# Optimization experiments

Hardware: AMD Instinct MI355X
Metric: run time of the kernel (lower is better)

## Reference

```python
import jax, jax.numpy as jnp
import numpy as np

N = 8192  # number of observations (rows of configuration)
D = 128   # embedding dimension


def _pair_indices(n):
    """Pair ordering of the original TF loop: for upper in 2..n-1, lower in 0..upper-1.
    (Pair (0,1) is never emitted by the original code.)"""
    counts = np.arange(2, n, dtype=np.int64)          # block u contributes u pairs
    uppers = np.repeat(counts, counts)
    starts = np.concatenate([np.zeros(1, np.int64), np.cumsum(counts)[:-1]])
    lowers = np.arange(uppers.shape[0], dtype=np.int64) - np.repeat(starts, counts)
    return lowers.astype(np.int32), uppers.astype(np.int32)


def setup_inputs() -> dict:
    key = jax.random.key(0)
    inputs = jax.random.normal(key, (N, D), dtype=jnp.float32)
    return {"inputs": inputs}


def reference(inputs):
    n = inputs.shape[0]
    lowers, uppers = _pair_indices(n)  # static (numpy) index arrays
    # trace(X^T (e_l-e_u)(e_l-e_u)^T X) == ||x_l - x_u||^2
    # Gram trick: ||x_l - x_u||^2 = ||x_l||^2 + ||x_u||^2 - 2 <x_l, x_u>
    sq = jnp.sum(inputs * inputs, axis=1)          # [n]
    gram = inputs @ inputs.T                        # [n, n]
    dists = sq[lowers] + sq[uppers] - 2.0 * gram[lowers, uppers]
    # Original TensorArray has size (n^2-n)/2 but only (n^2-n)/2 - 1 slots are
    # written (pair (0,1) is skipped); the last slot stacks as zero.
    out = jnp.concatenate([dists, jnp.zeros((1,), dists.dtype)])
    return out[None, :]  # tf.expand_dims(..., 0)
```

## Files before the change

kernel.cpp:

```cpp
#include <hip/hip_runtime.h>
#include <hip/hip_bf16.h>

#define NROWS 8192
#define DIM   128
#define NT    64
#define NBLK  (NT * (NT + 1) / 2)
#define TOTAL_OUT 33550336u

typedef short bf16x8 __attribute__((ext_vector_type(8)));
typedef float f32x4  __attribute__((ext_vector_type(4)));
typedef unsigned short u16x8 __attribute__((ext_vector_type(8)));

static __device__ inline unsigned short f32_to_bf16(float f) {
    unsigned int u = __float_as_uint(f);
    u += 0x7FFFu + ((u >> 16) & 1u);
    return (unsigned short)(u >> 16);
}

__global__ __launch_bounds__(256) void prep_kernel(const float* __restrict__ X,
                                                   unsigned short* __restrict__ Xr,
                                                   float* __restrict__ sq,
                                                   float* __restrict__ out) {
    __shared__ float sm[16][17];
    const int g = blockIdx.x;
    const int t = threadIdx.x;
    const int kk = t >> 6, lane = t & 63;
    const int lrow = lane & 15, kgrp = lane >> 4;

    const float* src = X + (size_t)(g * 16 + lrow) * DIM + (kk * 4 + kgrp) * 8;
    const float4 v0 = *reinterpret_cast<const float4*>(src);
    const float4 v1 = *reinterpret_cast<const float4*>(src + 4);

    u16x8 h;
    h[0] = f32_to_bf16(v0.x); h[1] = f32_to_bf16(v0.y);
    h[2] = f32_to_bf16(v0.z); h[3] = f32_to_bf16(v0.w);
    h[4] = f32_to_bf16(v1.x); h[5] = f32_to_bf16(v1.y);
    h[6] = f32_to_bf16(v1.z); h[7] = f32_to_bf16(v1.w);
    *reinterpret_cast<u16x8*>(Xr + ((size_t)(g * 4 + kk) * 64 + lane) * 8) = h;

    float p = v0.x * v0.x + v0.y * v0.y + v0.z * v0.z + v0.w * v0.w
            + v1.x * v1.x + v1.y * v1.y + v1.z * v1.z + v1.w * v1.w;
    sm[lrow][kk * 4 + kgrp] = p;
    __syncthreads();
    if (t < 16) {
        float s = 0.f;
        #pragma unroll
        for (int j = 0; j < 16; ++j) s += sm[t][j];
        sq[g * 16 + t] = s;
    }
    if (g == 0 && t == 0) out[TOTAL_OUT - 1] = 0.0f;
}

__global__ __launch_bounds__(256, 4) void pdist_kernel(const unsigned short* __restrict__ Xr,
                                                       const float* __restrict__ sq,
                                                       float* __restrict__ out) {
    const int t  = threadIdx.x;
    const int bt = blockIdx.x;
    int bj = (int)((sqrtf(8.0f * (float)bt + 1.0f) - 1.0f) * 0.5f);
    while ((bj + 1) * (bj + 2) / 2 <= bt) ++bj;
    while (bj * (bj + 1) / 2 > bt) --bj;
    const int bi = bt - bj * (bj + 1) / 2;

    const int wid  = t >> 6;
    const int lane = t & 63;
    const int wr   = wid >> 1;
    const int wc   = wid & 1;
    const int lrow = lane & 15;
    const int kgrp = lane >> 4;

    const bf16x8* __restrict__ F = reinterpret_cast<const bf16x8*>(Xr);
    const int gA = bi * 8 + wr * 4;
    const int gB = bj * 8 + wc * 4;

    f32x4 acc[4][4];
    const f32x4 fzero = {0.f, 0.f, 0.f, 0.f};
    #pragma unroll
    for (int m = 0; m < 4; ++m)
        #pragma unroll
        for (int n = 0; n < 4; ++n) acc[m][n] = fzero;

    bf16x8 a[2][4], b[2][4];
    #pragma unroll
    for (int m = 0; m < 4; ++m) {
        a[0][m] = F[((gA + m) * 4 + 0) * 64 + lane];
        b[0][m] = F[((gB + m) * 4 + 0) * 64 + lane];
    }
    #pragma unroll
    for (int kk = 0; kk < 4; ++kk) {
        const int cur = kk & 1, nxt = cur ^ 1;
        if (kk < 3) {
            #pragma unroll
            for (int m = 0; m < 4; ++m) {
                a[nxt][m] = F[((gA + m) * 4 + kk + 1) * 64 + lane];
                b[nxt][m] = F[((gB + m) * 4 + kk + 1) * 64 + lane];
            }
        }
        #pragma unroll
        for (int m = 0; m < 4; ++m)
            #pragma unroll
            for (int n = 0; n < 4; ++n)
                acc[m][n] = __builtin_amdgcn_mfma_f32_16x16x32_bf16(a[cur][m], b[cur][n], acc[m][n], 0, 0, 0);
    }

    const int l0 = bi * 128 + wr * 64;
    const int u0 = bj * 128 + wc * 64;
    const int rj = kgrp * 4;

    float squ[4];
    f32x4 sql[4];
    #pragma unroll
    for (int n = 0; n < 4; ++n) squ[n] = sq[u0 + n * 16 + lrow];
    #pragma unroll
    for (int m = 0; m < 4; ++m)
        sql[m] = *reinterpret_cast<const f32x4*>(sq + l0 + m * 16 + rj);

    if (bi != bj) {
        #pragma unroll
        for (int m = 0; m < 4; ++m) {
            #pragma unroll
            for (int n = 0; n < 4; ++n) {
                const int u = u0 + n * 16 + lrow;
                const size_t base = ((size_t)u * (u - 1)) / 2 - 1 + (size_t)(l0 + m * 16 + rj);
                f32x4 d;
                #pragma unroll
                for (int j = 0; j < 4; ++j) d[j] = sql[m][j] + squ[n] - 2.0f * acc[m][n][j];
                __builtin_memcpy(out + base, &d, 16);
            }
        }
    } else {
        #pragma unroll
        for (int m = 0; m < 4; ++m) {
            #pragma unroll
            for (int n = 0; n < 4; ++n) {
                const int u = u0 + n * 16 + lrow;
                #pragma unroll
                for (int j = 0; j < 4; ++j) {
                    const int l = l0 + m * 16 + rj + j;
                    if (l < u && u >= 2) {
                        out[((size_t)u * (u - 1)) / 2 - 1 + l] = sql[m][j] + squ[n] - 2.0f * acc[m][n][j];
                    }
                }
            }
        }
    }
}

extern "C" void kernel_launch(void* const* d_in, const int* in_sizes, int n_in,
                              void* d_out, int out_size, void* d_ws, size_t ws_size,
                              hipStream_t stream) {
    const float* X = (const float*)d_in[0];
    float* out = (float*)d_out;
    unsigned short* Xr = (unsigned short*)d_ws;
    float* sq = (float*)((char*)d_ws + (size_t)NROWS * DIM * 2);

    prep_kernel<<<NROWS / 16, 256, 0, stream>>>(X, Xr, sq, out);
    pdist_kernel<<<NBLK, 256, 0, stream>>>(Xr, sq, out);
}
```

Baseline: 54.08 us.

## Stage output tile in LDS for coalesced row stores with 256x64 tiles

Changes the block tiling from 128x128 to 256 lower rows by 64 upper columns and stages the distance tile through XOR-swizzled shared memory. Each wave can then write contiguous 1 KB segments of each packed output row instead of scattered 16-byte chunks. The aim is better write coalescing on a kernel dominated by its roughly 134 MB output. The cost is 32 KB of LDS per block plus two barriers, which may limit occupancy, and the diagonal tiles now use a simpler masked store path.

```diff
diff --git a/kernel.cpp b/kernel.cpp
--- a/kernel.cpp
+++ b/kernel.cpp
@@ -3,9 +3,8 @@
 
 #define NROWS 8192
 #define DIM   128
-#define NT    64
-#define NBLK  (NT * (NT + 1) / 2)
 #define TOTAL_OUT 33550336u
+#define NBLK2 2112
 
 typedef short bf16x8 __attribute__((ext_vector_type(8)));
 typedef float f32x4  __attribute__((ext_vector_type(4)));
@@ -15,6 +14,11 @@
     unsigned int u = __float_as_uint(f);
     u += 0x7FFFu + ((u >> 16) & 1u);
     return (unsigned short)(u >> 16);
+}
+
+static __device__ inline int cumtiles(int b) {
+    int q = b >> 2, r = b & 3;
+    return 2 * q * (q + 1) + r * (q + 1);
 }
 
 __global__ __launch_bounds__(256) void prep_kernel(const float* __restrict__ X,
@@ -54,23 +58,25 @@
 __global__ __launch_bounds__(256, 4) void pdist_kernel(const unsigned short* __restrict__ Xr,
                                                        const float* __restrict__ sq,
                                                        float* __restrict__ out) {
+    __shared__ f32x4 smC[32 * 64];
+
     const int t  = threadIdx.x;
     const int bt = blockIdx.x;
-    int bj = (int)((sqrtf(8.0f * (float)bt + 1.0f) - 1.0f) * 0.5f);
-    while ((bj + 1) * (bj + 2) / 2 <= bt) ++bj;
-    while (bj * (bj + 1) / 2 > bt) --bj;
-    const int bi = bt - bj * (bj + 1) / 2;
+    int bj = (int)sqrtf(8.0f * (float)bt + 1.0f);
+    if (bj > 127) bj = 127;
+    while (cumtiles(bj) > bt) --bj;
+    while (bj < 127 && cumtiles(bj + 1) <= bt) ++bj;
+    const int bi = bt - cumtiles(bj);
 
     const int wid  = t >> 6;
     const int lane = t & 63;
-    const int wr   = wid >> 1;
-    const int wc   = wid & 1;
+    const int wr   = wid;
     const int lrow = lane & 15;
     const int kgrp = lane >> 4;
 
     const bf16x8* __restrict__ F = reinterpret_cast<const bf16x8*>(Xr);
-    const int gA = bi * 8 + wr * 4;
-    const int gB = bj * 8 + wc * 4;
+    const int gA = bi * 16 + wr * 4;
+    const int gB = bj * 4;
 
     f32x4 acc[4][4];
     const f32x4 fzero = {0.f, 0.f, 0.f, 0.f};
@@ -102,9 +108,9 @@
                 acc[m][n] = __builtin_amdgcn_mfma_f32_16x16x32_bf16(a[cur][m], b[cur][n], acc[m][n], 0, 0, 0);
     }
 
-    const int l0 = bi * 128 + wr * 64;
-    const int u0 = bj * 128 + wc * 64;
-    const int rj = kgrp * 4;
+    const int u0  = bj * 64;
+    const int l0w = bi * 256 + wr * 64;
+    const bool diag = (bi == (bj >> 2));
 
     float squ[4];
     f32x4 sql[4];
@@ -112,33 +118,42 @@
     for (int n = 0; n < 4; ++n) squ[n] = sq[u0 + n * 16 + lrow];
     #pragma unroll
     for (int m = 0; m < 4; ++m)
-        sql[m] = *reinterpret_cast<const f32x4*>(sq + l0 + m * 16 + rj);
+        sql[m] = *reinterpret_cast<const f32x4*>(sq + l0w + m * 16 + kgrp * 4);
 
-    if (bi != bj) {
+    #pragma unroll
+    for (int h = 0; h < 2; ++h) {
+        if (h) __syncthreads();
         #pragma unroll
         for (int m = 0; m < 4; ++m) {
             #pragma unroll
-            for (int n = 0; n < 4; ++n) {
-                const int u = u0 + n * 16 + lrow;
-                const size_t base = ((size_t)u * (u - 1)) / 2 - 1 + (size_t)(l0 + m * 16 + rj);
+            for (int nn = 0; nn < 2; ++nn) {
+                const int n = 2 * h + nn;
+                const int u_loc = nn * 16 + lrow;
+                const int c = wr * 16 + m * 4 + kgrp;
                 f32x4 d;
                 #pragma unroll
                 for (int j = 0; j < 4; ++j) d[j] = sql[m][j] + squ[n] - 2.0f * acc[m][n][j];
-                __builtin_memcpy(out + base, &d, 16);
+                smC[u_loc * 64 + (c ^ lrow)] = d;
             }
         }
-    } else {
+        __syncthreads();
         #pragma unroll
-        for (int m = 0; m < 4; ++m) {
-            #pragma unroll
-            for (int n = 0; n < 4; ++n) {
-                const int u = u0 + n * 16 + lrow;
-                #pragma unroll
-                for (int j = 0; j < 4; ++j) {
-                    const int l = l0 + m * 16 + rj + j;
-                    if (l < u && u >= 2) {
-                        out[((size_t)u * (u - 1)) / 2 - 1 + l] = sql[m][j] + squ[n] - 2.0f * acc[m][n][j];
-                    }
+        for (int r8 = 0; r8 < 8; ++r8) {
+            const int u_loc = wid * 8 + r8;
+            const int u = u0 + 32 * h + u_loc;
+            const f32x4 v = smC[u_loc * 64 + (lane ^ (u_loc & 15))];
+            const size_t base = (size_t)u * (u - 1) / 2 - 1 + (size_t)bi * 256;
+            const int ll = lane * 4;
+            if (!diag) {
+                __builtin_memcpy(out + base + ll, &v, 16);
+            } else if (u >= 2) {
+                const int nvalid = u - bi * 256;
+                if (ll + 3 < nvalid) {
+                    __builtin_memcpy(out + base + ll, &v, 16);
+                } else {
+                    #pragma unroll
+                    for (int j = 0; j < 4; ++j)
+                        if (ll + j < nvalid) out[base + ll + j] = v[j];
                 }
             }
         }
@@ -154,5 +169,5 @@
     float* sq = (float*)((char*)d_ws + (size_t)NROWS * DIM * 2);
 
     prep_kernel<<<NROWS / 16, 256, 0, stream>>>(X, Xr, sq, out);
-    pdist_kernel<<<NBLK, 256, 0, stream>>>(Xr, sq, out);
+    pdist_kernel<<<NBLK2, 256, 0, stream>>>(Xr, sq, out);
 }
```

New measurement: 56.54 us. +4.5%, slower.

## Restructure pdist into row-strip blocks with LDS-staged contiguous output writes

Applied to the files above, without the earlier changes.

Replaces the triangular 128x128 tile grid with blocks that each own a 16-row strip of uppers and sweep across lower tiles, splitting long strips across 1-4 blocks for load balance. Gram results are staged through shared memory so each thread writes 8 contiguous floats along an output row, making stores coalesced along the packed triangular layout. This targets the scattered, strided stores of the original tile-wise writes, at the cost of two barriers per lower tile and less MFMA reuse per loaded operand, since each block computes only a 16x128 sub-tile per step.

```diff
diff --git a/kernel.cpp b/kernel.cpp
--- a/kernel.cpp
+++ b/kernel.cpp
@@ -3,9 +3,8 @@
 
 #define NROWS 8192
 #define DIM   128
-#define NT    64
-#define NBLK  (NT * (NT + 1) / 2)
 #define TOTAL_OUT 33550336u
+#define NBLK_P 1280
 
 typedef short bf16x8 __attribute__((ext_vector_type(8)));
 typedef float f32x4  __attribute__((ext_vector_type(4)));
@@ -51,97 +50,104 @@
     if (g == 0 && t == 0) out[TOTAL_OUT - 1] = 0.0f;
 }
 
-__global__ __launch_bounds__(256, 4) void pdist_kernel(const unsigned short* __restrict__ Xr,
+__global__ __launch_bounds__(256, 2) void pdist_kernel(const unsigned short* __restrict__ Xr,
                                                        const float* __restrict__ sq,
                                                        float* __restrict__ out) {
-    const int t  = threadIdx.x;
-    const int bt = blockIdx.x;
-    int bj = (int)((sqrtf(8.0f * (float)bt + 1.0f) - 1.0f) * 0.5f);
-    while ((bj + 1) * (bj + 2) / 2 <= bt) ++bj;
-    while (bj * (bj + 1) / 2 > bt) --bj;
-    const int bi = bt - bj * (bj + 1) / 2;
+    __shared__ float smC[16][132];
+
+    const int t   = threadIdx.x;
+    const int bid = blockIdx.x;
+    int g, part, np;
+    if (bid < 512)       { g = 511 - (bid >> 2);        part = bid & 3;  np = 4; }
+    else if (bid < 896)  { int q = bid - 512;  g = 383 - q / 3;  part = q % 3;  np = 3; }
+    else if (bid < 1152) { int q = bid - 896;  g = 255 - (q >> 1); part = q & 1; np = 2; }
+    else                 { g = 127 - (bid - 1152);      part = 0;      np = 1; }
+
+    const int ext = (16 * g + 14) / 128 + 1;
+    const int t0  = (ext * part) / np;
+    const int t1  = (ext * (part + 1)) / np;
 
     const int wid  = t >> 6;
     const int lane = t & 63;
-    const int wr   = wid >> 1;
-    const int wc   = wid & 1;
     const int lrow = lane & 15;
     const int kgrp = lane >> 4;
+    const bf16x8* __restrict__ F = reinterpret_cast<const bf16x8*>(Xr);
 
-    const bf16x8* __restrict__ F = reinterpret_cast<const bf16x8*>(Xr);
-    const int gA = bi * 8 + wr * 4;
-    const int gB = bj * 8 + wc * 4;
+    bf16x8 a[4];
+    #pragma unroll
+    for (int kk = 0; kk < 4; ++kk) a[kk] = F[(g * 4 + kk) * 64 + lane];
 
-    f32x4 acc[4][4];
-    const f32x4 fzero = {0.f, 0.f, 0.f, 0.f};
-    #pragma unroll
-    for (int m = 0; m < 4; ++m)
+    const int rr = t >> 4;
+    const int cc = (t & 15) * 8;
+    const int u_t = 16 * g + rr;
+    const float squ_t = sq[u_t];
+    const size_t base_u = (u_t >= 2) ? ((size_t)u_t * (size_t)(u_t - 1) / 2 - 1) : 0;
+
+    bf16x8 bA[2][4], bB[2][4];
+    auto loadB = [&](bf16x8 (&buf)[2][4], int lt) {
         #pragma unroll
-        for (int n = 0; n < 4; ++n) acc[m][n] = fzero;
+        for (int n = 0; n < 2; ++n)
+            #pragma unroll
+            for (int kk = 0; kk < 4; ++kk)
+                buf[n][kk] = F[((8 * lt + 2 * wid + n) * 4 + kk) * 64 + lane];
+    };
 
-    bf16x8 a[2][4], b[2][4];
-    #pragma unroll
-    for (int m = 0; m < 4; ++m) {
-        a[0][m] = F[((gA + m) * 4 + 0) * 64 + lane];
-        b[0][m] = F[((gB + m) * 4 + 0) * 64 + lane];
-    }
-    #pragma unroll
-    for (int kk = 0; kk < 4; ++kk) {
-        const int cur = kk & 1, nxt = cur ^ 1;
-        if (kk < 3) {
+    if (t0 < t1) loadB(bA, t0);
+    for (int lt = t0; lt < t1; ++lt) {
+        f32x4 acc[2];
+        acc[0] = (f32x4){0.f, 0.f, 0.f, 0.f};
+        acc[1] = (f32x4){0.f, 0.f, 0.f, 0.f};
+        if ((lt - t0) & 1) {
+            if (lt + 1 < t1) loadB(bA, lt + 1);
             #pragma unroll
-            for (int m = 0; m < 4; ++m) {
-                a[nxt][m] = F[((gA + m) * 4 + kk + 1) * 64 + lane];
-                b[nxt][m] = F[((gB + m) * 4 + kk + 1) * 64 + lane];
+            for (int kk = 0; kk < 4; ++kk) {
+                acc[0] = __builtin_amdgcn_mfma_f32_16x16x32_bf16(a[kk], bB[0][kk], acc[0], 0, 0, 0);
+                acc[1] = __builtin_amdgcn_mfma_f32_16x16x32_bf16(a[kk], bB[1][kk], acc[1], 0, 0, 0);
+            }
+        } else {
+            if (lt + 1 < t1) loadB(bB, lt + 1);
+            #pragma unroll
+            for (int kk = 0; kk < 4; ++kk) {
+                acc[0] = __builtin_amdgcn_mfma_f32_16x16x32_bf16(a[kk], bA[0][kk], acc[0], 0, 0, 0);
+                acc[1] = __builtin_amdgcn_mfma_f32_16x16x32_bf16(a[kk], bA[1][kk], acc[1], 0, 0, 0);
             }
         }
         #pragma unroll
-        for (int m = 0; m < 4; ++m)
+        for (int n = 0; n < 2; ++n)
             #pragma unroll
-            for (int n = 0; n < 4; ++n)
-                acc[m][n] = __builtin_amdgcn_mfma_f32_16x16x32_bf16(a[cur][m], b[cur][n], acc[m][n], 0, 0, 0);
-    }
-
-    const int l0 = bi * 128 + wr * 64;
-    const int u0 = bj * 128 + wc * 64;
-    const int rj = kgrp * 4;
-
-    float squ[4];
-    f32x4 sql[4];
-    #pragma unroll
-    for (int n = 0; n < 4; ++n) squ[n] = sq[u0 + n * 16 + lrow];
-    #pragma unroll
-    for (int m = 0; m < 4; ++m)
-        sql[m] = *reinterpret_cast<const f32x4*>(sq + l0 + m * 16 + rj);
-
-    if (bi != bj) {
-        #pragma unroll
-        for (int m = 0; m < 4; ++m) {
-            #pragma unroll
-            for (int n = 0; n < 4; ++n) {
-                const int u = u0 + n * 16 + lrow;
-                const size_t base = ((size_t)u * (u - 1)) / 2 - 1 + (size_t)(l0 + m * 16 + rj);
-                f32x4 d;
-                #pragma unroll
-                for (int j = 0; j < 4; ++j) d[j] = sql[m][j] + squ[n] - 2.0f * acc[m][n][j];
-                __builtin_memcpy(out + base, &d, 16);
-            }
-        }
-    } else {
-        #pragma unroll
-        for (int m = 0; m < 4; ++m) {
-            #pragma unroll
-            for (int n = 0; n < 4; ++n) {
-                const int u = u0 + n * 16 + lrow;
-                #pragma unroll
-                for (int j = 0; j < 4; ++j) {
-                    const int l = l0 + m * 16 + rj + j;
-                    if (l < u && u >= 2) {
-                        out[((size_t)u * (u - 1)) / 2 - 1 + l] = sql[m][j] + squ[n] - 2.0f * acc[m][n][j];
+            for (int j = 0; j < 4; ++j)
+                smC[kgrp * 4 + j][wid * 32 + n * 16 + lrow] = acc[n][j];
+        __syncthreads();
+        {
+            const int l0 = lt * 128 + cc;
+            if (u_t >= 2 && l0 < u_t) {
+                const float* srow = &smC[rr][cc];
+                const f32x4 v0 = *reinterpret_cast<const f32x4*>(srow);
+                const f32x4 v1 = *reinterpret_cast<const f32x4*>(srow + 4);
+                if (l0 + 7 < u_t) {
+                    const f32x4 s0 = *reinterpret_cast<const f32x4*>(sq + l0);
+                    const f32x4 s1 = *reinterpret_cast<const f32x4*>(sq + l0 + 4);
+                    f32x4 d0, d1;
+                    #pragma unroll
+                    for (int i = 0; i < 4; ++i) {
+                        d0[i] = squ_t + s0[i] - 2.0f * v0[i];
+                        d1[i] = squ_t + s1[i] - 2.0f * v1[i];
+                    }
+                    __builtin_memcpy(out + base_u + l0, &d0, 16);
+                    __builtin_memcpy(out + base_u + l0 + 4, &d1, 16);
+                } else {
+                    #pragma unroll
+                    for (int i = 0; i < 8; ++i) {
+                        const int l = l0 + i;
+                        if (l < u_t) {
+                            const float v = (i < 4) ? v0[i] : v1[i - 4];
+                            out[base_u + l] = squ_t + sq[l] - 2.0f * v;
+                        }
                     }
                 }
             }
         }
+        __syncthreads();
     }
 }
 
@@ -154,5 +160,5 @@
     float* sq = (float*)((char*)d_ws + (size_t)NROWS * DIM * 2);
 
     prep_kernel<<<NROWS / 16, 256, 0, stream>>>(X, Xr, sq, out);
-    pdist_kernel<<<NBLK, 256, 0, stream>>>(Xr, sq, out);
+    pdist_kernel<<<NBLK_P, 256, 0, stream>>>(Xr, sq, out);
 }
```

Measured after the change: 59.81 us. 10.6% more time.

## Stage pdist tile through swizzled LDS for aligned row-contiguous output stores

Applied to the files above, without the earlier changes.

The output epilogue now writes each half of the 128x128 distance tile into a swizzled shared-memory buffer, then has four threads per output row copy contiguous row segments to global memory with 16-byte aligned vector stores plus scalar head and tail. This replaces the scattered, mostly misaligned memcpy stores and the per-element masked diagonal path, targeting better write coalescing on this store-bound kernel. Block indices are also remapped in an interleaved order to spread neighbouring tiles across XCDs. The change adds 32KB of LDS per block, two barriers, and drops the occupancy hint in launch_bounds, which may reduce occupancy.

```diff
diff --git a/kernel.cpp b/kernel.cpp
--- a/kernel.cpp
+++ b/kernel.cpp
@@ -15,6 +15,10 @@
     unsigned int u = __float_as_uint(f);
     u += 0x7FFFu + ((u >> 16) & 1u);
     return (unsigned short)(u >> 16);
+}
+
+static __device__ inline int tidx(int row, int col) {
+    return row * 128 + ((((col >> 2) ^ (row & 7)) << 2) | (col & 3));
 }
 
 __global__ __launch_bounds__(256) void prep_kernel(const float* __restrict__ X,
@@ -51,11 +55,14 @@
     if (g == 0 && t == 0) out[TOTAL_OUT - 1] = 0.0f;
 }
 
-__global__ __launch_bounds__(256, 4) void pdist_kernel(const unsigned short* __restrict__ Xr,
-                                                       const float* __restrict__ sq,
-                                                       float* __restrict__ out) {
-    const int t  = threadIdx.x;
-    const int bt = blockIdx.x;
+__global__ __launch_bounds__(256) void pdist_kernel(const unsigned short* __restrict__ Xr,
+                                                    const float* __restrict__ sq,
+                                                    float* __restrict__ out) {
+    __shared__ float smT[64 * 128];
+
+    const int t    = threadIdx.x;
+    const int phys = blockIdx.x;
+    const int bt   = (phys & 7) * (NBLK / 8) + (phys >> 3);
     int bj = (int)((sqrtf(8.0f * (float)bt + 1.0f) - 1.0f) * 0.5f);
     while ((bj + 1) * (bj + 2) / 2 <= bt) ++bj;
     while (bj * (bj + 1) / 2 > bt) --bj;
@@ -104,7 +111,7 @@
 
     const int l0 = bi * 128 + wr * 64;
     const int u0 = bj * 128 + wc * 64;
-    const int rj = kgrp * 4;
+    const int l0blk = bi * 128;
 
     float squ[4];
     f32x4 sql[4];
@@ -112,33 +119,50 @@
     for (int n = 0; n < 4; ++n) squ[n] = sq[u0 + n * 16 + lrow];
     #pragma unroll
     for (int m = 0; m < 4; ++m)
-        sql[m] = *reinterpret_cast<const f32x4*>(sq + l0 + m * 16 + rj);
+        sql[m] = *reinterpret_cast<const f32x4*>(sq + l0 + m * 16 + kgrp * 4);
 
-    if (bi != bj) {
-        #pragma unroll
-        for (int m = 0; m < 4; ++m) {
+    #pragma unroll
+    for (int h = 0; h < 2; ++h) {
+        if (h) __syncthreads();
+        if (wc == h) {
             #pragma unroll
-            for (int n = 0; n < 4; ++n) {
-                const int u = u0 + n * 16 + lrow;
-                const size_t base = ((size_t)u * (u - 1)) / 2 - 1 + (size_t)(l0 + m * 16 + rj);
-                f32x4 d;
+            for (int m = 0; m < 4; ++m) {
                 #pragma unroll
-                for (int j = 0; j < 4; ++j) d[j] = sql[m][j] + squ[n] - 2.0f * acc[m][n][j];
-                __builtin_memcpy(out + base, &d, 16);
+                for (int n = 0; n < 4; ++n) {
+                    const int u_loc = n * 16 + lrow;
+                    const int l_loc = wr * 64 + m * 16 + kgrp * 4;
+                    f32x4 d;
+                    #pragma unroll
+                    for (int j = 0; j < 4; ++j) d[j] = sql[m][j] + squ[n] - 2.0f * acc[m][n][j];
+                    *reinterpret_cast<f32x4*>(&smT[tidx(u_loc, l_loc)]) = d;
+                }
             }
         }
-    } else {
-        #pragma unroll
-        for (int m = 0; m < 4; ++m) {
-            #pragma unroll
-            for (int n = 0; n < 4; ++n) {
-                const int u = u0 + n * 16 + lrow;
-                #pragma unroll
-                for (int j = 0; j < 4; ++j) {
-                    const int l = l0 + m * 16 + rj + j;
-                    if (l < u && u >= 2) {
-                        out[((size_t)u * (u - 1)) / 2 - 1 + l] = sql[m][j] + squ[n] - 2.0f * acc[m][n][j];
+        __syncthreads();
+        {
+            const int u_loc = t >> 2;
+            const int q = t & 3;
+            const int u = bj * 128 + h * 64 + u_loc;
+            if (u >= 2) {
+                int len = (bi != bj) ? 128 : (u - l0blk);
+                if (len > 128) len = 128;
+                if (len > 0) {
+                    const size_t B = (size_t)u * (size_t)(u - 1) / 2 - 1 + (size_t)l0blk;
+                    int h0 = (int)((4 - (B & 3)) & 3);
+                    if (h0 > len) h0 = len;
+                    const int body4 = (len - h0) >> 2;
+                    if (q == 0)
+                        for (int e = 0; e < h0; ++e) out[B + e] = smT[tidx(u_loc, e)];
+                    const int cend = ((q + 1) * 8 < body4) ? (q + 1) * 8 : body4;
+                    for (int c = q * 8; c < cend; ++c) {
+                        const int col = h0 + c * 4;
+                        f32x4 v;
+                        #pragma unroll
+                        for (int e = 0; e < 4; ++e) v[e] = smT[tidx(u_loc, col + e)];
+                        __builtin_memcpy(out + B + col, &v, 16);
                     }
+                    if (q == 3)
+                        for (int e = h0 + body4 * 4; e < len; ++e) out[B + e] = smT[tidx(u_loc, e)];
                 }
             }
         }
```

Measured after the change: 69.93 us. 1.29x slower.
